# Performance work log

Hardware: AMD Instinct MI355X
Metric: run time of the kernel (lower is better)

## Reference

```python
import jax, jax.numpy as jnp
import numpy as np

VOCAB, EMBED, HIDDEN, CH = 500, 80, 512, 128
B, L, T = 128, 784, 256


def setup_inputs() -> dict:
    key = jax.random.key(0)
    ks = jax.random.split(key, 14)
    s = lambda fan_in: 1.0 / np.sqrt(fan_in)
    return {
        "latent_rep": jax.random.normal(ks[0], (B, L, CH), jnp.float32),
        "formulas": jax.random.randint(ks[1], (B, T), 0, VOCAB),
        "embedding": jax.random.normal(ks[2], (VOCAB, EMBED), jnp.float32),
        "W_ih": jax.random.uniform(ks[3], (4 * HIDDEN, HIDDEN + EMBED), jnp.float32, -s(HIDDEN), s(HIDDEN)),
        "b_ih": jax.random.uniform(ks[4], (4 * HIDDEN,), jnp.float32, -s(HIDDEN), s(HIDDEN)),
        "W_hh": jax.random.uniform(ks[5], (4 * HIDDEN, HIDDEN), jnp.float32, -s(HIDDEN), s(HIDDEN)),
        "b_hh": jax.random.uniform(ks[6], (4 * HIDDEN,), jnp.float32, -s(HIDDEN), s(HIDDEN)),
        "Wh": jax.random.uniform(ks[7], (HIDDEN, CH), jnp.float32, -s(CH), s(CH)),
        "bh": jax.random.uniform(ks[8], (HIDDEN,), jnp.float32, -s(CH), s(CH)),
        "Wc": jax.random.uniform(ks[9], (HIDDEN, CH), jnp.float32, -s(CH), s(CH)),
        "bc": jax.random.uniform(ks[10], (HIDDEN,), jnp.float32, -s(CH), s(CH)),
        "Wo": jax.random.uniform(ks[11], (HIDDEN, CH), jnp.float32, -s(CH), s(CH)),
        "bo": jax.random.uniform(ks[12], (HIDDEN,), jnp.float32, -s(CH), s(CH)),
    }


def reference(latent_rep, formulas, embedding, W_ih, b_ih, W_hh, b_hh, Wh, bh, Wc, bc, Wo, bo):
    # init_lstm: tanh(Linear(mean over spatial positions))
    mean_lr = latent_rep.mean(axis=1)                       # [B, C]
    h0 = jnp.tanh(mean_lr @ Wh.T + bh)                       # [B, H]
    c0 = jnp.tanh(mean_lr @ Wc.T + bc)
    o0 = jnp.tanh(mean_lr @ Wo.T + bo)                       # fixed across steps in source

    emb = embedding[formulas]                                # [B, T, E]
    xs = jnp.swapaxes(emb, 0, 1)                             # [T, B, E]

    def step(carry, emb_t):
        h, c = carry
        inp = jnp.concatenate([o0, emb_t], axis=1)           # [B, H+E]
        gates = inp @ W_ih.T + b_ih + h @ W_hh.T + b_hh      # [B, 4H]
        i_g, f_g, g_g, o_g = jnp.split(gates, 4, axis=1)
        c_new = jax.nn.sigmoid(f_g) * c + jax.nn.sigmoid(i_g) * jnp.tanh(g_g)
        h_new = jax.nn.sigmoid(o_g) * jnp.tanh(c_new)
        # dropout in eval mode = identity
        return (h_new, c_new), h_new

    _, hs = jax.lax.scan(step, (h0, c0), xs)                 # hs: [T, B, H]
    return jnp.swapaxes(hs, 0, 1)                            # [B, T, H]
```

## Files before the change

kernel.cpp:

```cpp
#include <hip/hip_runtime.h>
#include <hip/hip_bf16.h>
#include <stdint.h>

typedef unsigned int uint32;
typedef unsigned long long uint64;
typedef __attribute__((ext_vector_type(8))) short short8;
typedef __attribute__((ext_vector_type(4))) float f32x4;

#define NB 128
#define NT 256
#define NH 512
#define NE 80
#define NCH 128
#define NL 784
#define NV 500
#define NG4 2048

#define HB_PAIRS (NB*(NH/2))

__device__ __forceinline__ unsigned short f2bf(float f){
  union { float f; unsigned int i; } v; v.f = f;
  unsigned int r = v.i + 0x7FFFu + ((v.i >> 16) & 1u);
  return (unsigned short)(r >> 16);
}
__device__ __forceinline__ float sigf(float x){ return 1.0f/(1.0f + __expf(-x)); }
__device__ __forceinline__ float tanhfast(float x){ return 1.0f - 2.0f/(__expf(2.0f*x)+1.0f); }

__global__ void k_mean(const float* __restrict__ lat, float* __restrict__ meanv){
  int b = blockIdx.x;
  int tid = threadIdx.x;
  int c4 = tid & 31;
  int part = tid >> 5;
  const float4* row = (const float4*)(lat + (size_t)b*NL*NCH);
  float sx=0.f, sy=0.f, sz=0.f, sw=0.f;
  for (int l=part; l<NL; l+=8){
    float4 v = row[l*32 + c4];
    sx+=v.x; sy+=v.y; sz+=v.z; sw+=v.w;
  }
  __shared__ float red[8][32][4];
  red[part][c4][0]=sx; red[part][c4][1]=sy; red[part][c4][2]=sz; red[part][c4][3]=sw;
  __syncthreads();
  if (part==0){
    float a0=0,a1=0,a2=0,a3=0;
    #pragma unroll
    for (int p=0;p<8;p++){ a0+=red[p][c4][0]; a1+=red[p][c4][1]; a2+=red[p][c4][2]; a3+=red[p][c4][3]; }
    float4 o; o.x=a0*(1.0f/NL); o.y=a1*(1.0f/NL); o.z=a2*(1.0f/NL); o.w=a3*(1.0f/NL);
    ((float4*)meanv)[b*32 + c4] = o;
  }
}

__global__ void k_init(const float* __restrict__ meanv,
    const float* __restrict__ Wh, const float* __restrict__ bh,
    const float* __restrict__ Wc, const float* __restrict__ bc,
    const float* __restrict__ Wo, const float* __restrict__ bo,
    float* __restrict__ c0, float* __restrict__ o0, uint64* __restrict__ hbuf){
  int b = blockIdx.x; int j = threadIdx.x;
  __shared__ unsigned short hsh[NH];
  const float* m = meanv + b*NCH;
  const float4* wh = (const float4*)(Wh + (size_t)j*NCH);
  const float4* wc = (const float4*)(Wc + (size_t)j*NCH);
  const float4* wo = (const float4*)(Wo + (size_t)j*NCH);
  float sh=0.f, sc=0.f, so=0.f;
  for (int c=0; c<NCH/4; c++){
    float4 vh = wh[c], vc = wc[c], vo = wo[c];
    float m0=m[c*4], m1=m[c*4+1], m2=m[c*4+2], m3=m[c*4+3];
    sh += m0*vh.x + m1*vh.y + m2*vh.z + m3*vh.w;
    sc += m0*vc.x + m1*vc.y + m2*vc.z + m3*vc.w;
    so += m0*vo.x + m1*vo.y + m2*vo.z + m3*vo.w;
  }
  float h0 = tanhf(sh + bh[j]);
  c0[b*NH+j] = tanhf(sc + bc[j]);
  o0[b*NH+j] = tanhf(so + bo[j]);
  hsh[j] = f2bf(h0);
  __syncthreads();
  if (j < NH/2){
    uint32 packed = (uint32)hsh[2*j] | ((uint32)hsh[2*j+1] << 16);
    hbuf[(size_t)b*(NH/2) + j] = (uint64)packed;
  }
}

__global__ void k_table(const float* __restrict__ emb,
                        const float* __restrict__ Wih,
                        float* __restrict__ table){
  int v = blockIdx.x;
  int n = blockIdx.y*256 + threadIdx.x;
  const float4* wr = (const float4*)(Wih + (size_t)n*(NH+NE) + NH);
  const float4* er = (const float4*)(emb + v*NE);
  float s = 0.f;
  for (int e4=0; e4<NE/4; e4++){
    float4 w = wr[e4], e = er[e4];
    s += w.x*e.x + w.y*e.y + w.z*e.z + w.w*e.w;
  }
  table[(size_t)v*NG4 + n] = s;
}

__global__ void k_base(const float* __restrict__ o0,
                       const float* __restrict__ Wih,
                       const float* __restrict__ bih,
                       const float* __restrict__ bhh,
                       float* __restrict__ base){
  int b = blockIdx.x;
  int n = blockIdx.y*256 + threadIdx.x;
  const float4* o = (const float4*)(o0 + b*NH);
  const float4* wr = (const float4*)(Wih + (size_t)n*(NH+NE));
  float s = bih[n] + bhh[n];
  for (int k4=0;k4<NH/4;k4++){
    float4 w = wr[k4], v = o[k4];
    s += w.x*v.x + w.y*v.y + w.z*v.z + w.w*v.w;
  }
  base[(size_t)b*NG4 + n] = s;
}

__global__ __launch_bounds__(256, 1) void k_lstm(
    const float* __restrict__ Whh,
    const int* __restrict__ formulas,
    const float* __restrict__ table,
    const float* __restrict__ base,
    const float* __restrict__ c0,
    uint64* hbuf,
    float* __restrict__ out)
{
  int bid = blockIdx.x;
  int g = bid & 7, s = bid >> 3;
  int tid = threadIdx.x;
  int lane = tid & 63, w = tid >> 6;
  int b0 = g*16, u0 = s*32;

  __shared__ __align__(16) char h_lds[16*1024];
  __shared__ float G[16*132 + 4];

  short8 bw[2][16];
  {
    int krow = (lane >> 4) * 8;
    #pragma unroll
    for (int h2=0; h2<2; h2++){
      int c_loc = w*32 + h2*16 + (lane & 15);
      int wrow = (c_loc >> 5)*NH + u0 + (c_loc & 31);
      const float4* p4 = (const float4*)(Whh + (size_t)wrow*NH + krow);
      #pragma unroll
      for (int ks=0; ks<16; ks++){
        float4 lo = p4[ks*8], hi = p4[ks*8+1];
        short8 t;
        t[0]=(short)f2bf(lo.x); t[1]=(short)f2bf(lo.y); t[2]=(short)f2bf(lo.z); t[3]=(short)f2bf(lo.w);
        t[4]=(short)f2bf(hi.x); t[5]=(short)f2bf(hi.y); t[6]=(short)f2bf(hi.z); t[7]=(short)f2bf(hi.w);
        bw[h2][ks] = t;
      }
    }
  }

  int r_e = tid >> 4, up = tid & 15;
  int be = b0 + r_e;
  float cst0 = c0[be*NH + u0 + 2*up];
  float cst1 = c0[be*NH + u0 + 2*up + 1];

  float2 bsv[4];
  #pragma unroll
  for (int gt=0; gt<4; gt++)
    bsv[gt] = *(const float2*)(base + (size_t)be*NG4 + gt*NH + u0 + 2*up);

  float2 tbv[4];
  {
    int tok0 = formulas[be*NT + 0];
    #pragma unroll
    for (int gt=0; gt<4; gt++)
      tbv[gt] = *(const float2*)(table + (size_t)tok0*NG4 + gt*NH + u0 + 2*up);
  }

  int arow = lane & 15;
  int abyte = arow*1024 + ((lane>>4)*8)*2;
  int aswz = (arow & 7) << 4;

  for (int t=0; t<NT; t++){
    uint64* hrd = hbuf + (size_t)(t & 1)*HB_PAIRS;
    uint64* hwr = hbuf + (size_t)((t+1) & 1)*HB_PAIRS;
    const uint32 etag = (uint32)t;

    uint64 vv[16];
    #pragma unroll
    for (int i=0;i<16;i++)
      vv[i] = __hip_atomic_load(&hrd[(size_t)b0*(NH/2) + tid + i*256],
                                __ATOMIC_RELAXED, __HIP_MEMORY_SCOPE_AGENT);
    uint32 stale = 0;
    #pragma unroll
    for (int i=0;i<16;i++) if ((uint32)(vv[i] >> 32) != etag) stale |= 1u << i;
    int guard = 0;
    while (stale && ++guard < (1<<16)){
      #pragma unroll
      for (int i=0;i<16;i++) if (stale & (1u << i))
        vv[i] = __hip_atomic_load(&hrd[(size_t)b0*(NH/2) + tid + i*256],
                                  __ATOMIC_RELAXED, __HIP_MEMORY_SCOPE_AGENT);
      stale = 0;
      #pragma unroll
      for (int i=0;i<16;i++) if ((uint32)(vv[i] >> 32) != etag) stale |= 1u << i;
    }

    #pragma unroll
    for (int i=0;i<16;i++){
      int p = tid + i*256;
      int r = p >> 8, cu = p & 255;
      *(uint32*)(h_lds + ((r*1024 + cu*4) ^ ((r & 7) << 4))) = (uint32)vv[i];
    }
    __syncthreads();

    f32x4 acc0 = {0.f,0.f,0.f,0.f}, acc1 = {0.f,0.f,0.f,0.f};
    #pragma unroll
    for (int ks=0; ks<16; ks++){
      short8 a = *(const short8*)(h_lds + ((abyte + ks*64) ^ aswz));
      acc0 = __builtin_amdgcn_mfma_f32_16x16x32_bf16(a, bw[0][ks], acc0, 0, 0, 0);
      acc1 = __builtin_amdgcn_mfma_f32_16x16x32_bf16(a, bw[1][ks], acc1, 0, 0, 0);
    }

    {
      int rbase = (lane>>4)*4;
      int col0 = (w*2+0)*16 + (lane&15);
      int col1 = (w*2+1)*16 + (lane&15);
      #pragma unroll
      for (int r4=0;r4<4;r4++){
        G[(rbase+r4)*132 + col0] = acc0[r4];
        G[(rbase+r4)*132 + col1] = acc1[r4];
      }
    }
    __syncthreads();

    float hn0, hn1;
    {
      const float* Gr = G + r_e*132 + 2*up;
      float gi0 = Gr[0]   + tbv[0].x + bsv[0].x;
      float gi1 = Gr[1]   + tbv[0].y + bsv[0].y;
      float gf0 = Gr[32]  + tbv[1].x + bsv[1].x;
      float gf1 = Gr[33]  + tbv[1].y + bsv[1].y;
      float gg0 = Gr[64]  + tbv[2].x + bsv[2].x;
      float gg1 = Gr[65]  + tbv[2].y + bsv[2].y;
      float go0 = Gr[96]  + tbv[3].x + bsv[3].x;
      float go1 = Gr[97]  + tbv[3].y + bsv[3].y;
      float cn0 = sigf(gf0)*cst0 + sigf(gi0)*tanhfast(gg0);
      float cn1 = sigf(gf1)*cst1 + sigf(gi1)*tanhfast(gg1);
      cst0 = cn0; cst1 = cn1;
      hn0 = sigf(go0)*tanhfast(cn0);
      hn1 = sigf(go1)*tanhfast(cn1);
    }

    if (t < NT-1){
      uint32 packed = (uint32)f2bf(hn0) | ((uint32)f2bf(hn1) << 16);
      uint64 pv = (uint64)packed | ((uint64)(uint32)(t+1) << 32);
      __hip_atomic_store(&hwr[(size_t)be*(NH/2) + (u0/2 + up)], pv,
                         __ATOMIC_RELAXED, __HIP_MEMORY_SCOPE_AGENT);
    }

    {
      float2 ov; ov.x = hn0; ov.y = hn1;
      *(float2*)(out + ((size_t)be*NT + t)*NH + u0 + 2*up) = ov;
    }
    if (t < NT-1){
      int tokn = formulas[be*NT + t + 1];
      #pragma unroll
      for (int gt=0; gt<4; gt++)
        tbv[gt] = *(const float2*)(table + (size_t)tokn*NG4 + gt*NH + u0 + 2*up);
    }
  }
}

extern "C" void kernel_launch(void* const* d_in, const int* in_sizes, int n_in,
                              void* d_out, int out_size, void* d_ws, size_t ws_size,
                              hipStream_t stream) {
  const float* lat      = (const float*)d_in[0];
  const int*   formulas = (const int*)d_in[1];
  const float* emb      = (const float*)d_in[2];
  const float* Wih      = (const float*)d_in[3];
  const float* bih      = (const float*)d_in[4];
  const float* Whh      = (const float*)d_in[5];
  const float* bhh      = (const float*)d_in[6];
  const float* Wh       = (const float*)d_in[7];
  const float* bh       = (const float*)d_in[8];
  const float* Wc       = (const float*)d_in[9];
  const float* bc       = (const float*)d_in[10];
  const float* Wo       = (const float*)d_in[11];
  const float* bo       = (const float*)d_in[12];
  float* out = (float*)d_out;

  char* ws = (char*)d_ws;
  float* meanv = (float*)ws;  ws += (size_t)NB*NCH*4;
  float* c0    = (float*)ws;  ws += (size_t)NB*NH*4;
  float* o0    = (float*)ws;  ws += (size_t)NB*NH*4;
  float* table = (float*)ws;  ws += (size_t)NV*NG4*4;
  float* base  = (float*)ws;  ws += (size_t)NB*NG4*4;
  uint64* hbuf = (uint64*)ws; ws += (size_t)2*HB_PAIRS*8;

  hipMemsetAsync(hbuf, 0, (size_t)2*HB_PAIRS*8, stream);
  k_mean <<<NB, 256, 0, stream>>>(lat, meanv);
  k_init <<<NB, NH, 0, stream>>>(meanv, Wh, bh, Wc, bc, Wo, bo, c0, o0, hbuf);
  k_table<<<dim3(NV, 8), 256, 0, stream>>>(emb, Wih, table);
  k_base <<<dim3(NB, 8), 256, 0, stream>>>(o0, Wih, bih, bhh, base);
  k_lstm <<<NB, 256, 0, stream>>>(Whh, formulas, table, base, c0, hbuf, out);
}
```

Before: 740.7 us.

## Feed MFMA directly from tagged global h loads, dropping LDS staging and barriers

The persistent LSTM kernel now uses 128 threads per block. Each wave computes all four gates for 16 units, so the gate nonlinearity runs straight from the MFMA accumulators and the G shared-memory transpose goes away. The hidden state is stored as 32-bit words holding a bf16 value plus a 16-bit step tag. Each lane loads its MFMA A-operand fragments straight from global memory and spins per k-chunk until the tags match, which removes the LDS staging and both __syncthreads per step. Loads start at a block-rotated k offset and are prefetched one chunk ahead to overlap polling with the matrix multiplies. In exchange, each wave issues more fine-grained atomic loads, the 16-bit tag only covers up to 65535 steps, and bf16 precision per element is unchanged.

```diff
diff --git a/kernel.cpp b/kernel.cpp
--- a/kernel.cpp
+++ b/kernel.cpp
@@ -15,8 +15,6 @@
 #define NL 784
 #define NV 500
 #define NG4 2048
-
-#define HB_PAIRS (NB*(NH/2))
 
 __device__ __forceinline__ unsigned short f2bf(float f){
   union { float f; unsigned int i; } v; v.f = f;
@@ -53,9 +51,8 @@
     const float* __restrict__ Wh, const float* __restrict__ bh,
     const float* __restrict__ Wc, const float* __restrict__ bc,
     const float* __restrict__ Wo, const float* __restrict__ bo,
-    float* __restrict__ c0, float* __restrict__ o0, uint64* __restrict__ hbuf){
+    float* __restrict__ c0, float* __restrict__ o0, uint32* __restrict__ hbuf){
   int b = blockIdx.x; int j = threadIdx.x;
-  __shared__ unsigned short hsh[NH];
   const float* m = meanv + b*NCH;
   const float4* wh = (const float4*)(Wh + (size_t)j*NCH);
   const float4* wc = (const float4*)(Wc + (size_t)j*NCH);
@@ -71,12 +68,7 @@
   float h0 = tanhf(sh + bh[j]);
   c0[b*NH+j] = tanhf(sc + bc[j]);
   o0[b*NH+j] = tanhf(so + bo[j]);
-  hsh[j] = f2bf(h0);
-  __syncthreads();
-  if (j < NH/2){
-    uint32 packed = (uint32)hsh[2*j] | ((uint32)hsh[2*j+1] << 16);
-    hbuf[(size_t)b*(NH/2) + j] = (uint64)packed;
-  }
+  hbuf[(size_t)b*NH + j] = (uint32)f2bf(h0);
 }
 
 __global__ void k_table(const float* __restrict__ emb,
@@ -111,13 +103,13 @@
   base[(size_t)b*NG4 + n] = s;
 }
 
-__global__ __launch_bounds__(256, 1) void k_lstm(
+__global__ __launch_bounds__(128, 1) void k_lstm(
     const float* __restrict__ Whh,
     const int* __restrict__ formulas,
     const float* __restrict__ table,
     const float* __restrict__ base,
     const float* __restrict__ c0,
-    uint64* hbuf,
+    uint32* hbuf,
     float* __restrict__ out)
 {
   int bid = blockIdx.x;
@@ -125,137 +117,129 @@
   int tid = threadIdx.x;
   int lane = tid & 63, w = tid >> 6;
   int b0 = g*16, u0 = s*32;
-
-  __shared__ __align__(16) char h_lds[16*1024];
-  __shared__ float G[16*132 + 4];
-
-  short8 bw[2][16];
+  int col = lane & 15;
+  int hi  = lane >> 4;
+  int myunit = u0 + w*16 + col;
+  int r0 = hi*4;
+
+  short8 bwf0[16], bwf1[16], bwf2[16], bwf3[16];
   {
-    int krow = (lane >> 4) * 8;
-    #pragma unroll
-    for (int h2=0; h2<2; h2++){
-      int c_loc = w*32 + h2*16 + (lane & 15);
-      int wrow = (c_loc >> 5)*NH + u0 + (c_loc & 31);
-      const float4* p4 = (const float4*)(Whh + (size_t)wrow*NH + krow);
+    #pragma unroll
+    for (int j=0;j<16;j++){
+      int ksd = (j + s) & 15;
+      int kof = ksd*32 + hi*8;
       #pragma unroll
-      for (int ks=0; ks<16; ks++){
-        float4 lo = p4[ks*8], hi = p4[ks*8+1];
-        short8 t;
-        t[0]=(short)f2bf(lo.x); t[1]=(short)f2bf(lo.y); t[2]=(short)f2bf(lo.z); t[3]=(short)f2bf(lo.w);
-        t[4]=(short)f2bf(hi.x); t[5]=(short)f2bf(hi.y); t[6]=(short)f2bf(hi.z); t[7]=(short)f2bf(hi.w);
-        bw[h2][ks] = t;
-      }
-    }
-  }
-
-  int r_e = tid >> 4, up = tid & 15;
-  int be = b0 + r_e;
-  float cst0 = c0[be*NH + u0 + 2*up];
-  float cst1 = c0[be*NH + u0 + 2*up + 1];
-
-  float2 bsv[4];
+      for (int gt=0; gt<4; gt++){
+        const float4* p4 = (const float4*)(Whh + (size_t)(gt*NH + myunit)*NH + kof);
+        float4 lo = p4[0], hp = p4[1];
+        short8 tv;
+        tv[0]=(short)f2bf(lo.x); tv[1]=(short)f2bf(lo.y); tv[2]=(short)f2bf(lo.z); tv[3]=(short)f2bf(lo.w);
+        tv[4]=(short)f2bf(hp.x); tv[5]=(short)f2bf(hp.y); tv[6]=(short)f2bf(hp.z); tv[7]=(short)f2bf(hp.w);
+        if (gt==0) bwf0[j]=tv; else if (gt==1) bwf1[j]=tv; else if (gt==2) bwf2[j]=tv; else bwf3[j]=tv;
+      }
+    }
+  }
+
+  float cst[4];
+  float bs[4][4], tb[4][4];
   #pragma unroll
-  for (int gt=0; gt<4; gt++)
-    bsv[gt] = *(const float2*)(base + (size_t)be*NG4 + gt*NH + u0 + 2*up);
-
-  float2 tbv[4];
-  {
+  for (int r=0;r<4;r++){
+    int be = b0 + r0 + r;
+    cst[r] = c0[be*NH + myunit];
+    #pragma unroll
+    for (int gt=0; gt<4; gt++)
+      bs[r][gt] = base[(size_t)be*NG4 + gt*NH + myunit];
     int tok0 = formulas[be*NT + 0];
     #pragma unroll
     for (int gt=0; gt<4; gt++)
-      tbv[gt] = *(const float2*)(table + (size_t)tok0*NG4 + gt*NH + u0 + 2*up);
-  }
-
-  int arow = lane & 15;
-  int abyte = arow*1024 + ((lane>>4)*8)*2;
-  int aswz = (arow & 7) << 4;
+      tb[r][gt] = table[(size_t)tok0*NG4 + gt*NH + myunit];
+  }
+
+  int abase = (b0 + col)*(NH/2) + hi*4;
 
   for (int t=0; t<NT; t++){
-    uint64* hrd = hbuf + (size_t)(t & 1)*HB_PAIRS;
-    uint64* hwr = hbuf + (size_t)((t+1) & 1)*HB_PAIRS;
+    const uint64* hrd64 = (const uint64*)(hbuf + (size_t)(t & 1)*NB*NH);
+    uint64*       hwr64 = (uint64*)      (hbuf + (size_t)((t+1) & 1)*NB*NH);
     const uint32 etag = (uint32)t;
 
-    uint64 vv[16];
-    #pragma unroll
-    for (int i=0;i<16;i++)
-      vv[i] = __hip_atomic_load(&hrd[(size_t)b0*(NH/2) + tid + i*256],
-                                __ATOMIC_RELAXED, __HIP_MEMORY_SCOPE_AGENT);
-    uint32 stale = 0;
-    #pragma unroll
-    for (int i=0;i<16;i++) if ((uint32)(vv[i] >> 32) != etag) stale |= 1u << i;
-    int guard = 0;
-    while (stale && ++guard < (1<<16)){
+    uint64 vv[16][4];
+    #define LOADC(j_) { int ksd = ((j_) + s) & 15;                                   \
+      const uint64* p_ = hrd64 + abase + ksd*16;                                     \
+      vv[j_][0] = __hip_atomic_load(p_+0, __ATOMIC_RELAXED, __HIP_MEMORY_SCOPE_AGENT); \
+      vv[j_][1] = __hip_atomic_load(p_+1, __ATOMIC_RELAXED, __HIP_MEMORY_SCOPE_AGENT); \
+      vv[j_][2] = __hip_atomic_load(p_+2, __ATOMIC_RELAXED, __HIP_MEMORY_SCOPE_AGENT); \
+      vv[j_][3] = __hip_atomic_load(p_+3, __ATOMIC_RELAXED, __HIP_MEMORY_SCOPE_AGENT); }
+    #define TAGDIFF(j_) (((((uint32)(vv[j_][0] >> 16)) ^ etag) & 0xFFFFu) |          \
+                         ((((uint32)(vv[j_][1] >> 16)) ^ etag) & 0xFFFFu) |          \
+                         ((((uint32)(vv[j_][2] >> 16)) ^ etag) & 0xFFFFu) |          \
+                         ((((uint32)(vv[j_][3] >> 16)) ^ etag) & 0xFFFFu))
+
+    #pragma unroll
+    for (int j=0;j<8;j++) LOADC(j);
+
+    f32x4 acc0 = {0.f,0.f,0.f,0.f}, acc1 = {0.f,0.f,0.f,0.f};
+    f32x4 acc2 = {0.f,0.f,0.f,0.f}, acc3 = {0.f,0.f,0.f,0.f};
+
+    #pragma unroll
+    for (int j=0;j<16;j++){
+      uint32 d = TAGDIFF(j);
+      int guard = 0;
+      while (!__all(d == 0)){
+        LOADC(j);
+        d = TAGDIFF(j);
+        if (++guard > (1<<14)) break;
+      }
+      if (j < 8) LOADC(j+8);
+      uint32 a0 = __builtin_amdgcn_perm((uint32)(vv[j][0] >> 32), (uint32)vv[j][0], 0x05040100u);
+      uint32 a1 = __builtin_amdgcn_perm((uint32)(vv[j][1] >> 32), (uint32)vv[j][1], 0x05040100u);
+      uint32 a2 = __builtin_amdgcn_perm((uint32)(vv[j][2] >> 32), (uint32)vv[j][2], 0x05040100u);
+      uint32 a3 = __builtin_amdgcn_perm((uint32)(vv[j][3] >> 32), (uint32)vv[j][3], 0x05040100u);
+      union { uint32 u[4]; short8 s8; } af;
+      af.u[0]=a0; af.u[1]=a1; af.u[2]=a2; af.u[3]=a3;
+      acc0 = __builtin_amdgcn_mfma_f32_16x16x32_bf16(af.s8, bwf0[j], acc0, 0, 0, 0);
+      acc1 = __builtin_amdgcn_mfma_f32_16x16x32_bf16(af.s8, bwf1[j], acc1, 0, 0, 0);
+      acc2 = __builtin_amdgcn_mfma_f32_16x16x32_bf16(af.s8, bwf2[j], acc2, 0, 0, 0);
+      acc3 = __builtin_amdgcn_mfma_f32_16x16x32_bf16(af.s8, bwf3[j], acc3, 0, 0, 0);
+    }
+    #undef LOADC
+    #undef TAGDIFF
+
+    #pragma unroll
+    for (int r=0;r<4;r++){
+      int be = b0 + r0 + r;
+      float gi = acc0[r] + tb[r][0] + bs[r][0];
+      float gf = acc1[r] + tb[r][1] + bs[r][1];
+      float gg = acc2[r] + tb[r][2] + bs[r][2];
+      float go = acc3[r] + tb[r][3] + bs[r][3];
+      float cn = sigf(gf)*cst[r] + sigf(gi)*tanhfast(gg);
+      cst[r] = cn;
+      float hn = sigf(go)*tanhfast(cn);
+
+      if (t < NT-1){
+        uint32 tagged = ((uint32)(t+1) << 16) | (uint32)f2bf(hn);
+        uint32 ptag = (uint32)__shfl_xor((int)tagged, 1);
+        if ((lane & 1) == 0){
+          uint64 pv = (uint64)tagged | ((uint64)ptag << 32);
+          __hip_atomic_store(hwr64 + (((size_t)be*NH + myunit) >> 1), pv,
+                             __ATOMIC_RELAXED, __HIP_MEMORY_SCOPE_AGENT);
+        }
+      }
+      float ph = __shfl_xor(hn, 1);
+      if ((lane & 1) == 0){
+        float2 ov; ov.x = hn; ov.y = ph;
+        *(float2*)(out + ((size_t)be*NT + t)*NH + myunit) = ov;
+      }
+    }
+
+    if (t < NT-1){
       #pragma unroll
-      for (int i=0;i<16;i++) if (stale & (1u << i))
-        vv[i] = __hip_atomic_load(&hrd[(size_t)b0*(NH/2) + tid + i*256],
-                                  __ATOMIC_RELAXED, __HIP_MEMORY_SCOPE_AGENT);
-      stale = 0;
-      #pragma unroll
-      for (int i=0;i<16;i++) if ((uint32)(vv[i] >> 32) != etag) stale |= 1u << i;
-    }
-
-    #pragma unroll
-    for (int i=0;i<16;i++){
-      int p = tid + i*256;
-      int r = p >> 8, cu = p & 255;
-      *(uint32*)(h_lds + ((r*1024 + cu*4) ^ ((r & 7) << 4))) = (uint32)vv[i];
-    }
-    __syncthreads();
-
-    f32x4 acc0 = {0.f,0.f,0.f,0.f}, acc1 = {0.f,0.f,0.f,0.f};
-    #pragma unroll
-    for (int ks=0; ks<16; ks++){
-      short8 a = *(const short8*)(h_lds + ((abyte + ks*64) ^ aswz));
-      acc0 = __builtin_amdgcn_mfma_f32_16x16x32_bf16(a, bw[0][ks], acc0, 0, 0, 0);
-      acc1 = __builtin_amdgcn_mfma_f32_16x16x32_bf16(a, bw[1][ks], acc1, 0, 0, 0);
-    }
-
-    {
-      int rbase = (lane>>4)*4;
-      int col0 = (w*2+0)*16 + (lane&15);
-      int col1 = (w*2+1)*16 + (lane&15);
-      #pragma unroll
-      for (int r4=0;r4<4;r4++){
-        G[(rbase+r4)*132 + col0] = acc0[r4];
-        G[(rbase+r4)*132 + col1] = acc1[r4];
-      }
-    }
-    __syncthreads();
-
-    float hn0, hn1;
-    {
-      const float* Gr = G + r_e*132 + 2*up;
-      float gi0 = Gr[0]   + tbv[0].x + bsv[0].x;
-      float gi1 = Gr[1]   + tbv[0].y + bsv[0].y;
-      float gf0 = Gr[32]  + tbv[1].x + bsv[1].x;
-      float gf1 = Gr[33]  + tbv[1].y + bsv[1].y;
-      float gg0 = Gr[64]  + tbv[2].x + bsv[2].x;
-      float gg1 = Gr[65]  + tbv[2].y + bsv[2].y;
-      float go0 = Gr[96]  + tbv[3].x + bsv[3].x;
-      float go1 = Gr[97]  + tbv[3].y + bsv[3].y;
-      float cn0 = sigf(gf0)*cst0 + sigf(gi0)*tanhfast(gg0);
-      float cn1 = sigf(gf1)*cst1 + sigf(gi1)*tanhfast(gg1);
-      cst0 = cn0; cst1 = cn1;
-      hn0 = sigf(go0)*tanhfast(cn0);
-      hn1 = sigf(go1)*tanhfast(cn1);
-    }
-
-    if (t < NT-1){
-      uint32 packed = (uint32)f2bf(hn0) | ((uint32)f2bf(hn1) << 16);
-      uint64 pv = (uint64)packed | ((uint64)(uint32)(t+1) << 32);
-      __hip_atomic_store(&hwr[(size_t)be*(NH/2) + (u0/2 + up)], pv,
-                         __ATOMIC_RELAXED, __HIP_MEMORY_SCOPE_AGENT);
-    }
-
-    {
-      float2 ov; ov.x = hn0; ov.y = hn1;
-      *(float2*)(out + ((size_t)be*NT + t)*NH + u0 + 2*up) = ov;
-    }
-    if (t < NT-1){
-      int tokn = formulas[be*NT + t + 1];
-      #pragma unroll
-      for (int gt=0; gt<4; gt++)
-        tbv[gt] = *(const float2*)(table + (size_t)tokn*NG4 + gt*NH + u0 + 2*up);
+      for (int r=0;r<4;r++){
+        int be = b0 + r0 + r;
+        int tokn = formulas[be*NT + t + 1];
+        #pragma unroll
+        for (int gt=0; gt<4; gt++)
+          tb[r][gt] = table[(size_t)tokn*NG4 + gt*NH + myunit];
+      }
     }
   }
 }
@@ -284,12 +268,12 @@
   float* o0    = (float*)ws;  ws += (size_t)NB*NH*4;
   float* table = (float*)ws;  ws += (size_t)NV*NG4*4;
   float* base  = (float*)ws;  ws += (size_t)NB*NG4*4;
-  uint64* hbuf = (uint64*)ws; ws += (size_t)2*HB_PAIRS*8;
-
-  hipMemsetAsync(hbuf, 0, (size_t)2*HB_PAIRS*8, stream);
+  uint32* hbuf = (uint32*)ws; ws += (size_t)2*NB*NH*4;
+
+  hipMemsetAsync(hbuf, 0, (size_t)2*NB*NH*4, stream);
   k_mean <<<NB, 256, 0, stream>>>(lat, meanv);
   k_init <<<NB, NH, 0, stream>>>(meanv, Wh, bh, Wc, bc, Wo, bo, c0, o0, hbuf);
   k_table<<<dim3(NV, 8), 256, 0, stream>>>(emb, Wih, table);
   k_base <<<dim3(NB, 8), 256, 0, stream>>>(o0, Wih, bih, bhh, base);
-  k_lstm <<<NB, 256, 0, stream>>>(Whh, formulas, table, base, c0, hbuf, out);
-}
+  k_lstm <<<NB, 128, 0, stream>>>(Whh, formulas, table, base, c0, hbuf, out);
+}
```

New measurement: 1.797 ms. 143% more time.

## Replace per-step block barrier with per-k-slice LDS ready flags in LSTM

Applied to the files above, without the earlier changes.

Reorganizes the cross-block hidden-state exchange buffer into per-k-slice tiles with a 16-bit step tag inside each bf16 value. Each wave polls and loads only its own k-slices, then publishes each slice to LDS with a workgroup release flag. The MFMA loop starts on locally held slices while other waves' slices arrive. The G buffer is double-buffered so one barrier per step can be dropped. The aim is to overlap the global polling latency with MFMA work and shorten the per-timestep critical path, at the cost of spin-loops on LDS flags and a more complex tagging scheme.

```diff
diff --git a/kernel.cpp b/kernel.cpp
--- a/kernel.cpp
+++ b/kernel.cpp
@@ -16,7 +16,7 @@
 #define NV 500
 #define NG4 2048
 
-#define HB_PAIRS (NB*(NH/2))
+#define HB64 (8*16*256)
 
 __device__ __forceinline__ unsigned short f2bf(float f){
   union { float f; unsigned int i; } v; v.f = f;
@@ -74,8 +74,9 @@
   hsh[j] = f2bf(h0);
   __syncthreads();
   if (j < NH/2){
-    uint32 packed = (uint32)hsh[2*j] | ((uint32)hsh[2*j+1] << 16);
-    hbuf[(size_t)b*(NH/2) + j] = (uint64)packed;
+    int g = b >> 4, r = b & 15, cs = j >> 4;
+    uint64 pv = (uint64)(uint32)hsh[2*j] | ((uint64)(uint32)hsh[2*j+1] << 32);
+    hbuf[(size_t)(g*16 + cs)*256 + r*16 + (j & 15)] = pv;
   }
 }
 
@@ -125,25 +126,31 @@
   int tid = threadIdx.x;
   int lane = tid & 63, w = tid >> 6;
   int b0 = g*16, u0 = s*32;
+  int row = lane & 15, hi = lane >> 4;
+  int slot = hi ^ (row & 3);
 
   __shared__ __align__(16) char h_lds[16*1024];
-  __shared__ float G[16*132 + 4];
-
-  short8 bw[2][16];
+  __shared__ float G[2][16*132 + 4];
+  __shared__ int ready[16];
+
+  if (tid < 16) ready[tid] = -1;
+
+  short8 bw_ord[2][16];
   {
-    int krow = (lane >> 4) * 8;
-    #pragma unroll
-    for (int h2=0; h2<2; h2++){
-      int c_loc = w*32 + h2*16 + (lane & 15);
-      int wrow = (c_loc >> 5)*NH + u0 + (c_loc & 31);
-      const float4* p4 = (const float4*)(Whh + (size_t)wrow*NH + krow);
-      #pragma unroll
-      for (int ks=0; ks<16; ks++){
-        float4 lo = p4[ks*8], hi = p4[ks*8+1];
-        short8 t;
-        t[0]=(short)f2bf(lo.x); t[1]=(short)f2bf(lo.y); t[2]=(short)f2bf(lo.z); t[3]=(short)f2bf(lo.w);
-        t[4]=(short)f2bf(hi.x); t[5]=(short)f2bf(hi.y); t[6]=(short)f2bf(hi.z); t[7]=(short)f2bf(hi.w);
-        bw[h2][ks] = t;
+    #pragma unroll
+    for (int jj=0; jj<16; jj++){
+      int ks = (w + (jj>>2) + 4*(jj&3)) & 15;
+      int kof = ks*32 + hi*8;
+      #pragma unroll
+      for (int h2=0; h2<2; h2++){
+        int c_loc = w*32 + h2*16 + row;
+        int wrow = (c_loc >> 5)*NH + u0 + (c_loc & 31);
+        const float4* p4 = (const float4*)(Whh + (size_t)wrow*NH + kof);
+        float4 lo = p4[0], hp = p4[1];
+        short8 tv;
+        tv[0]=(short)f2bf(lo.x); tv[1]=(short)f2bf(lo.y); tv[2]=(short)f2bf(lo.z); tv[3]=(short)f2bf(lo.w);
+        tv[4]=(short)f2bf(hp.x); tv[5]=(short)f2bf(hp.y); tv[6]=(short)f2bf(hp.z); tv[7]=(short)f2bf(hp.w);
+        bw_ord[h2][jj] = tv;
       }
     }
   }
@@ -166,65 +173,84 @@
       tbv[gt] = *(const float2*)(table + (size_t)tok0*NG4 + gt*NH + u0 + 2*up);
   }
 
-  int arow = lane & 15;
-  int abyte = arow*1024 + ((lane>>4)*8)*2;
-  int aswz = (arow & 7) << 4;
+  __syncthreads();
 
   for (int t=0; t<NT; t++){
-    uint64* hrd = hbuf + (size_t)(t & 1)*HB_PAIRS;
-    uint64* hwr = hbuf + (size_t)((t+1) & 1)*HB_PAIRS;
-    const uint32 etag = (uint32)t;
-
-    uint64 vv[16];
-    #pragma unroll
-    for (int i=0;i<16;i++)
-      vv[i] = __hip_atomic_load(&hrd[(size_t)b0*(NH/2) + tid + i*256],
-                                __ATOMIC_RELAXED, __HIP_MEMORY_SCOPE_AGENT);
-    uint32 stale = 0;
-    #pragma unroll
-    for (int i=0;i<16;i++) if ((uint32)(vv[i] >> 32) != etag) stale |= 1u << i;
-    int guard = 0;
-    while (stale && ++guard < (1<<16)){
-      #pragma unroll
-      for (int i=0;i<16;i++) if (stale & (1u << i))
-        vv[i] = __hip_atomic_load(&hrd[(size_t)b0*(NH/2) + tid + i*256],
-                                  __ATOMIC_RELAXED, __HIP_MEMORY_SCOPE_AGENT);
-      stale = 0;
-      #pragma unroll
-      for (int i=0;i<16;i++) if ((uint32)(vv[i] >> 32) != etag) stale |= 1u << i;
-    }
-
-    #pragma unroll
-    for (int i=0;i<16;i++){
-      int p = tid + i*256;
-      int r = p >> 8, cu = p & 255;
-      *(uint32*)(h_lds + ((r*1024 + cu*4) ^ ((r & 7) << 4))) = (uint32)vv[i];
-    }
-    __syncthreads();
+    const uint64* hrd64 = hbuf + (size_t)(t & 1)*HB64;
+    uint64*       hwr64 = hbuf + (size_t)((t+1) & 1)*HB64;
+    const uint32 etag = (uint32)t & 0xFFFFu;
+    int par = t & 1;
+
+    uint64 q[4][4];
+    #pragma unroll
+    for (int jj=0; jj<4; jj++){
+      int ks = (w + 4*jj) & 15;
+      const uint64* p = hrd64 + (size_t)(g*16 + ks)*256 + row*16 + hi*4;
+      #pragma unroll
+      for (int k=0;k<4;k++)
+        q[jj][k] = __hip_atomic_load(p+k, __ATOMIC_RELAXED, __HIP_MEMORY_SCOPE_AGENT);
+    }
+    short8 paf[4];
+    #pragma unroll
+    for (int jj=0; jj<4; jj++){
+      int ks = (w + 4*jj) & 15;
+      const uint64* p = hrd64 + (size_t)(g*16 + ks)*256 + row*16 + hi*4;
+      uint32 d = 0;
+      #pragma unroll
+      for (int k=0;k<4;k++) d |= (((uint32)(q[jj][k] >> 16)) ^ etag) & 0xFFFFu;
+      int guard = 0;
+      while (!__all(d == 0)){
+        #pragma unroll
+        for (int k=0;k<4;k++)
+          q[jj][k] = __hip_atomic_load(p+k, __ATOMIC_RELAXED, __HIP_MEMORY_SCOPE_AGENT);
+        d = 0;
+        #pragma unroll
+        for (int k=0;k<4;k++) d |= (((uint32)(q[jj][k] >> 16)) ^ etag) & 0xFFFFu;
+        if (++guard > (1<<16)) break;
+      }
+      union { uint32 u[4]; short8 s8; } af;
+      #pragma unroll
+      for (int k=0;k<4;k++)
+        af.u[k] = __builtin_amdgcn_perm((uint32)(q[jj][k] >> 32), (uint32)q[jj][k], 0x05040100u);
+      paf[jj] = af.s8;
+      *(short8*)(h_lds + ks*1024 + row*64 + slot*16) = af.s8;
+      __hip_atomic_store(&ready[ks], t, __ATOMIC_RELEASE, __HIP_MEMORY_SCOPE_WORKGROUP);
+    }
 
     f32x4 acc0 = {0.f,0.f,0.f,0.f}, acc1 = {0.f,0.f,0.f,0.f};
     #pragma unroll
-    for (int ks=0; ks<16; ks++){
-      short8 a = *(const short8*)(h_lds + ((abyte + ks*64) ^ aswz));
-      acc0 = __builtin_amdgcn_mfma_f32_16x16x32_bf16(a, bw[0][ks], acc0, 0, 0, 0);
-      acc1 = __builtin_amdgcn_mfma_f32_16x16x32_bf16(a, bw[1][ks], acc1, 0, 0, 0);
+    for (int jj=0; jj<16; jj++){
+      int ks = (w + (jj>>2) + 4*(jj&3)) & 15;
+      short8 a;
+      if (jj < 4){
+        a = paf[jj];
+      } else {
+        int guard = 0;
+        while (__hip_atomic_load(&ready[ks], __ATOMIC_ACQUIRE, __HIP_MEMORY_SCOPE_WORKGROUP) < t){
+          if (++guard > (1<<20)) break;
+        }
+        a = *(const short8*)(h_lds + ks*1024 + row*64 + slot*16);
+      }
+      acc0 = __builtin_amdgcn_mfma_f32_16x16x32_bf16(a, bw_ord[0][jj], acc0, 0, 0, 0);
+      acc1 = __builtin_amdgcn_mfma_f32_16x16x32_bf16(a, bw_ord[1][jj], acc1, 0, 0, 0);
     }
 
     {
-      int rbase = (lane>>4)*4;
-      int col0 = (w*2+0)*16 + (lane&15);
-      int col1 = (w*2+1)*16 + (lane&15);
+      float* Gp = G[par];
+      int rbase = hi*4;
+      int col0 = (w*2+0)*16 + row;
+      int col1 = (w*2+1)*16 + row;
       #pragma unroll
       for (int r4=0;r4<4;r4++){
-        G[(rbase+r4)*132 + col0] = acc0[r4];
-        G[(rbase+r4)*132 + col1] = acc1[r4];
+        Gp[(rbase+r4)*132 + col0] = acc0[r4];
+        Gp[(rbase+r4)*132 + col1] = acc1[r4];
       }
     }
     __syncthreads();
 
     float hn0, hn1;
     {
-      const float* Gr = G + r_e*132 + 2*up;
+      const float* Gr = G[par] + r_e*132 + 2*up;
       float gi0 = Gr[0]   + tbv[0].x + bsv[0].x;
       float gi1 = Gr[1]   + tbv[0].y + bsv[0].y;
       float gf0 = Gr[32]  + tbv[1].x + bsv[1].x;
@@ -241,9 +267,9 @@
     }
 
     if (t < NT-1){
-      uint32 packed = (uint32)f2bf(hn0) | ((uint32)f2bf(hn1) << 16);
-      uint64 pv = (uint64)packed | ((uint64)(uint32)(t+1) << 32);
-      __hip_atomic_store(&hwr[(size_t)be*(NH/2) + (u0/2 + up)], pv,
+      uint64 pv = ((uint64)(((uint32)(t+1) << 16) | (uint32)f2bf(hn0)))
+                | ((uint64)(((uint32)(t+1) << 16) | (uint32)f2bf(hn1)) << 32);
+      __hip_atomic_store(hwr64 + (size_t)(g*16 + s)*256 + tid, pv,
                          __ATOMIC_RELAXED, __HIP_MEMORY_SCOPE_AGENT);
     }
 
@@ -284,9 +310,9 @@
   float* o0    = (float*)ws;  ws += (size_t)NB*NH*4;
   float* table = (float*)ws;  ws += (size_t)NV*NG4*4;
   float* base  = (float*)ws;  ws += (size_t)NB*NG4*4;
-  uint64* hbuf = (uint64*)ws; ws += (size_t)2*HB_PAIRS*8;
-
-  hipMemsetAsync(hbuf, 0, (size_t)2*HB_PAIRS*8, stream);
+  uint64* hbuf = (uint64*)ws; ws += (size_t)2*HB64*8;
+
+  hipMemsetAsync(hbuf, 0, (size_t)2*HB64*8, stream);
   k_mean <<<NB, 256, 0, stream>>>(lat, meanv);
   k_init <<<NB, NH, 0, stream>>>(meanv, Wh, bh, Wc, bc, Wo, bo, c0, o0, hbuf);
   k_table<<<dim3(NV, 8), 256, 0, stream>>>(emb, Wih, table);
```

Measured after the change: 1.225 ms. 65.4% more time.

## Halve LSTM grid so each block processes two batch groups per step

Applied to the files above, without the earlier changes.

The persistent LSTM kernel now runs on 64 blocks instead of 128. Each block handles two 16-row batch groups in sequence inside every timestep, reusing the same register-resident W_hh slice, so half as many blocks take part in the cross-block spin synchronisation. The hidden-state exchange format also changes: each bf16 value is now packed with its own 16-bit step tag in a 64-bit word, which may be aimed at closing a torn-read hazard. The cost is that each block does twice as much serial work per step, on half the compute units.

```diff
diff --git a/kernel.cpp b/kernel.cpp
--- a/kernel.cpp
+++ b/kernel.cpp
@@ -74,8 +74,8 @@
   hsh[j] = f2bf(h0);
   __syncthreads();
   if (j < NH/2){
-    uint32 packed = (uint32)hsh[2*j] | ((uint32)hsh[2*j+1] << 16);
-    hbuf[(size_t)b*(NH/2) + j] = (uint64)packed;
+    uint64 pv = (uint64)(uint32)hsh[2*j] | ((uint64)(uint32)hsh[2*j+1] << 32);
+    hbuf[(size_t)b*(NH/2) + j] = pv;
   }
 }
 
@@ -121,10 +121,10 @@
     float* __restrict__ out)
 {
   int bid = blockIdx.x;
-  int g = bid & 7, s = bid >> 3;
+  int p = bid & 3, s = bid >> 2;
   int tid = threadIdx.x;
   int lane = tid & 63, w = tid >> 6;
-  int b0 = g*16, u0 = s*32;
+  int b0p = p*32, u0 = s*32;
 
   __shared__ __align__(16) char h_lds[16*1024];
   __shared__ float G[16*132 + 4];
@@ -149,21 +149,21 @@
   }
 
   int r_e = tid >> 4, up = tid & 15;
-  int be = b0 + r_e;
-  float cst0 = c0[be*NH + u0 + 2*up];
-  float cst1 = c0[be*NH + u0 + 2*up + 1];
-
-  float2 bsv[4];
+
+  float cst0[2], cst1[2];
+  float2 bsv[2][4], tbv[2][4];
   #pragma unroll
-  for (int gt=0; gt<4; gt++)
-    bsv[gt] = *(const float2*)(base + (size_t)be*NG4 + gt*NH + u0 + 2*up);
-
-  float2 tbv[4];
-  {
+  for (int ph=0; ph<2; ph++){
+    int be = b0p + ph*16 + r_e;
+    cst0[ph] = c0[be*NH + u0 + 2*up];
+    cst1[ph] = c0[be*NH + u0 + 2*up + 1];
+    #pragma unroll
+    for (int gt=0; gt<4; gt++)
+      bsv[ph][gt] = *(const float2*)(base + (size_t)be*NG4 + gt*NH + u0 + 2*up);
     int tok0 = formulas[be*NT + 0];
     #pragma unroll
     for (int gt=0; gt<4; gt++)
-      tbv[gt] = *(const float2*)(table + (size_t)tok0*NG4 + gt*NH + u0 + 2*up);
+      tbv[ph][gt] = *(const float2*)(table + (size_t)tok0*NG4 + gt*NH + u0 + 2*up);
   }
 
   int arow = lane & 15;
@@ -171,91 +171,102 @@
   int aswz = (arow & 7) << 4;
 
   for (int t=0; t<NT; t++){
-    uint64* hrd = hbuf + (size_t)(t & 1)*HB_PAIRS;
-    uint64* hwr = hbuf + (size_t)((t+1) & 1)*HB_PAIRS;
+    const uint64* hrdb = hbuf + (size_t)(t & 1)*HB_PAIRS;
+    uint64*       hwrb = hbuf + (size_t)((t+1) & 1)*HB_PAIRS;
     const uint32 etag = (uint32)t;
 
-    uint64 vv[16];
-    #pragma unroll
-    for (int i=0;i<16;i++)
-      vv[i] = __hip_atomic_load(&hrd[(size_t)b0*(NH/2) + tid + i*256],
-                                __ATOMIC_RELAXED, __HIP_MEMORY_SCOPE_AGENT);
-    uint32 stale = 0;
-    #pragma unroll
-    for (int i=0;i<16;i++) if ((uint32)(vv[i] >> 32) != etag) stale |= 1u << i;
-    int guard = 0;
-    while (stale && ++guard < (1<<16)){
-      #pragma unroll
-      for (int i=0;i<16;i++) if (stale & (1u << i))
-        vv[i] = __hip_atomic_load(&hrd[(size_t)b0*(NH/2) + tid + i*256],
+    #pragma unroll
+    for (int ph=0; ph<2; ph++){
+      int b0 = b0p + ph*16;
+      int be = b0 + r_e;
+
+      uint64 vv[16];
+      #pragma unroll
+      for (int i=0;i<16;i++)
+        vv[i] = __hip_atomic_load(&hrdb[(size_t)b0*(NH/2) + tid + i*256],
                                   __ATOMIC_RELAXED, __HIP_MEMORY_SCOPE_AGENT);
-      stale = 0;
-      #pragma unroll
-      for (int i=0;i<16;i++) if ((uint32)(vv[i] >> 32) != etag) stale |= 1u << i;
-    }
-
-    #pragma unroll
-    for (int i=0;i<16;i++){
-      int p = tid + i*256;
-      int r = p >> 8, cu = p & 255;
-      *(uint32*)(h_lds + ((r*1024 + cu*4) ^ ((r & 7) << 4))) = (uint32)vv[i];
-    }
-    __syncthreads();
-
-    f32x4 acc0 = {0.f,0.f,0.f,0.f}, acc1 = {0.f,0.f,0.f,0.f};
-    #pragma unroll
-    for (int ks=0; ks<16; ks++){
-      short8 a = *(const short8*)(h_lds + ((abyte + ks*64) ^ aswz));
-      acc0 = __builtin_amdgcn_mfma_f32_16x16x32_bf16(a, bw[0][ks], acc0, 0, 0, 0);
-      acc1 = __builtin_amdgcn_mfma_f32_16x16x32_bf16(a, bw[1][ks], acc1, 0, 0, 0);
-    }
-
-    {
-      int rbase = (lane>>4)*4;
-      int col0 = (w*2+0)*16 + (lane&15);
-      int col1 = (w*2+1)*16 + (lane&15);
-      #pragma unroll
-      for (int r4=0;r4<4;r4++){
-        G[(rbase+r4)*132 + col0] = acc0[r4];
-        G[(rbase+r4)*132 + col1] = acc1[r4];
-      }
-    }
-    __syncthreads();
-
-    float hn0, hn1;
-    {
-      const float* Gr = G + r_e*132 + 2*up;
-      float gi0 = Gr[0]   + tbv[0].x + bsv[0].x;
-      float gi1 = Gr[1]   + tbv[0].y + bsv[0].y;
-      float gf0 = Gr[32]  + tbv[1].x + bsv[1].x;
-      float gf1 = Gr[33]  + tbv[1].y + bsv[1].y;
-      float gg0 = Gr[64]  + tbv[2].x + bsv[2].x;
-      float gg1 = Gr[65]  + tbv[2].y + bsv[2].y;
-      float go0 = Gr[96]  + tbv[3].x + bsv[3].x;
-      float go1 = Gr[97]  + tbv[3].y + bsv[3].y;
-      float cn0 = sigf(gf0)*cst0 + sigf(gi0)*tanhfast(gg0);
-      float cn1 = sigf(gf1)*cst1 + sigf(gi1)*tanhfast(gg1);
-      cst0 = cn0; cst1 = cn1;
-      hn0 = sigf(go0)*tanhfast(cn0);
-      hn1 = sigf(go1)*tanhfast(cn1);
-    }
-
-    if (t < NT-1){
-      uint32 packed = (uint32)f2bf(hn0) | ((uint32)f2bf(hn1) << 16);
-      uint64 pv = (uint64)packed | ((uint64)(uint32)(t+1) << 32);
-      __hip_atomic_store(&hwr[(size_t)be*(NH/2) + (u0/2 + up)], pv,
-                         __ATOMIC_RELAXED, __HIP_MEMORY_SCOPE_AGENT);
-    }
-
-    {
-      float2 ov; ov.x = hn0; ov.y = hn1;
-      *(float2*)(out + ((size_t)be*NT + t)*NH + u0 + 2*up) = ov;
-    }
-    if (t < NT-1){
-      int tokn = formulas[be*NT + t + 1];
-      #pragma unroll
-      for (int gt=0; gt<4; gt++)
-        tbv[gt] = *(const float2*)(table + (size_t)tokn*NG4 + gt*NH + u0 + 2*up);
+      uint32 stale = 0;
+      #pragma unroll
+      for (int i=0;i<16;i++)
+        if ((((uint32)(vv[i] >> 16)) & 0xFFFFu) != (etag & 0xFFFFu) ||
+            (((uint32)(vv[i] >> 48)) & 0xFFFFu) != (etag & 0xFFFFu)) stale |= 1u << i;
+      int guard = 0;
+      while (stale && ++guard < (1<<16)){
+        #pragma unroll
+        for (int i=0;i<16;i++) if (stale & (1u << i))
+          vv[i] = __hip_atomic_load(&hrdb[(size_t)b0*(NH/2) + tid + i*256],
+                                    __ATOMIC_RELAXED, __HIP_MEMORY_SCOPE_AGENT);
+        stale = 0;
+        #pragma unroll
+        for (int i=0;i<16;i++)
+          if ((((uint32)(vv[i] >> 16)) & 0xFFFFu) != (etag & 0xFFFFu) ||
+              (((uint32)(vv[i] >> 48)) & 0xFFFFu) != (etag & 0xFFFFu)) stale |= 1u << i;
+      }
+
+      #pragma unroll
+      for (int i=0;i<16;i++){
+        int q = tid + i*256;
+        int r = q >> 8, cu = q & 255;
+        uint32 dw = __builtin_amdgcn_perm((uint32)(vv[i] >> 32), (uint32)vv[i], 0x05040100u);
+        *(uint32*)(h_lds + ((r*1024 + cu*4) ^ ((r & 7) << 4))) = dw;
+      }
+      __syncthreads();
+
+      f32x4 acc0 = {0.f,0.f,0.f,0.f}, acc1 = {0.f,0.f,0.f,0.f};
+      #pragma unroll
+      for (int ks=0; ks<16; ks++){
+        short8 a = *(const short8*)(h_lds + ((abyte + ks*64) ^ aswz));
+        acc0 = __builtin_amdgcn_mfma_f32_16x16x32_bf16(a, bw[0][ks], acc0, 0, 0, 0);
+        acc1 = __builtin_amdgcn_mfma_f32_16x16x32_bf16(a, bw[1][ks], acc1, 0, 0, 0);
+      }
+
+      {
+        int rbase = (lane>>4)*4;
+        int col0 = (w*2+0)*16 + (lane&15);
+        int col1 = (w*2+1)*16 + (lane&15);
+        #pragma unroll
+        for (int r4=0;r4<4;r4++){
+          G[(rbase+r4)*132 + col0] = acc0[r4];
+          G[(rbase+r4)*132 + col1] = acc1[r4];
+        }
+      }
+      __syncthreads();
+
+      float hn0, hn1;
+      {
+        const float* Gr = G + r_e*132 + 2*up;
+        float gi0 = Gr[0]   + tbv[ph][0].x + bsv[ph][0].x;
+        float gi1 = Gr[1]   + tbv[ph][0].y + bsv[ph][0].y;
+        float gf0 = Gr[32]  + tbv[ph][1].x + bsv[ph][1].x;
+        float gf1 = Gr[33]  + tbv[ph][1].y + bsv[ph][1].y;
+        float gg0 = Gr[64]  + tbv[ph][2].x + bsv[ph][2].x;
+        float gg1 = Gr[65]  + tbv[ph][2].y + bsv[ph][2].y;
+        float go0 = Gr[96]  + tbv[ph][3].x + bsv[ph][3].x;
+        float go1 = Gr[97]  + tbv[ph][3].y + bsv[ph][3].y;
+        float cn0 = sigf(gf0)*cst0[ph] + sigf(gi0)*tanhfast(gg0);
+        float cn1 = sigf(gf1)*cst1[ph] + sigf(gi1)*tanhfast(gg1);
+        cst0[ph] = cn0; cst1[ph] = cn1;
+        hn0 = sigf(go0)*tanhfast(cn0);
+        hn1 = sigf(go1)*tanhfast(cn1);
+      }
+
+      if (t < NT-1){
+        uint64 pv = ((uint64)(((uint32)(t+1) << 16) | (uint32)f2bf(hn0)))
+                  | ((uint64)(((uint32)(t+1) << 16) | (uint32)f2bf(hn1)) << 32);
+        __hip_atomic_store(&hwrb[(size_t)be*(NH/2) + (u0/2 + up)], pv,
+                           __ATOMIC_RELAXED, __HIP_MEMORY_SCOPE_AGENT);
+      }
+
+      {
+        float2 ov; ov.x = hn0; ov.y = hn1;
+        *(float2*)(out + ((size_t)be*NT + t)*NH + u0 + 2*up) = ov;
+      }
+      if (t < NT-1){
+        int tokn = formulas[be*NT + t + 1];
+        #pragma unroll
+        for (int gt=0; gt<4; gt++)
+          tbv[ph][gt] = *(const float2*)(table + (size_t)tokn*NG4 + gt*NH + u0 + 2*up);
+      }
     }
   }
 }
@@ -291,5 +302,5 @@
   k_init <<<NB, NH, 0, stream>>>(meanv, Wh, bh, Wc, bc, Wo, bo, c0, o0, hbuf);
   k_table<<<dim3(NV, 8), 256, 0, stream>>>(emb, Wih, table);
   k_base <<<dim3(NB, 8), 256, 0, stream>>>(o0, Wih, bih, bhh, base);
-  k_lstm <<<NB, 256, 0, stream>>>(Whh, formulas, table, base, c0, hbuf, out);
-}
+  k_lstm <<<64, 256, 0, stream>>>(Whh, formulas, table, base, c0, hbuf, out);
+}
```

After: 1.539 ms. 108% more time.
